# Optimization experiments

Measured on AMD Instinct MI355X. Metric: run time of the kernel, lower is better.

The kernel has to match this reference:

```python
import jax, jax.numpy as jnp
import numpy as np

B, S, D, H = 2, 2048, 1024, 16
DH = D // H
DFF = 4 * D
EPS = 1e-5


def layer_norm(x, w, b):
    m = jnp.mean(x, axis=-1, keepdims=True)
    v = jnp.mean((x - m) ** 2, axis=-1, keepdims=True)
    return (x - m) / jnp.sqrt(v + EPS) * w + b


def setup_inputs() -> dict:
    key = jax.random.key(0)
    ks = jax.random.split(key, 12)
    s = 0.02
    x = jax.random.normal(ks[0], (B, S, D), dtype=jnp.float32)
    mask = jnp.tril(jnp.ones((S, S), dtype=jnp.int32))  # causal mask, 0 = blocked
    Wq = jax.random.normal(ks[1], (H, D, DH), dtype=jnp.float32) * s
    Wk = jax.random.normal(ks[2], (H, D, DH), dtype=jnp.float32) * s
    Wv = jax.random.normal(ks[3], (H, D, DH), dtype=jnp.float32) * s
    Wo = jax.random.normal(ks[4], (D, D), dtype=jnp.float32) * s
    bo = jnp.zeros((D,), dtype=jnp.float32)
    W1 = jax.random.normal(ks[5], (D, DFF), dtype=jnp.float32) * s
    b1 = jnp.zeros((DFF,), dtype=jnp.float32)
    W2 = jax.random.normal(ks[6], (DFF, D), dtype=jnp.float32) * s
    b2 = jnp.zeros((D,), dtype=jnp.float32)
    ln1_w = jnp.ones((D,), dtype=jnp.float32)
    ln1_b = jnp.zeros((D,), dtype=jnp.float32)
    ln2_w = jnp.ones((D,), dtype=jnp.float32)
    ln2_b = jnp.zeros((D,), dtype=jnp.float32)
    return {"x": x, "mask": mask, "Wq": Wq, "Wk": Wk, "Wv": Wv, "Wo": Wo,
            "bo": bo, "W1": W1, "b1": b1, "W2": W2, "b2": b2,
            "ln1_w": ln1_w, "ln1_b": ln1_b, "ln2_w": ln2_w, "ln2_b": ln2_b}


def reference(x, mask, Wq, Wk, Wv, Wo, bo, W1, b1, W2, b2,
              ln1_w, ln1_b, ln2_w, ln2_b):
    # --- pre-LN attention ---
    xn = layer_norm(x, ln1_w, ln1_b)
    q = jnp.einsum('bsd,hdk->bhsk', xn, Wq)  # [B,H,S,DH]
    k = jnp.einsum('bsd,hdk->bhsk', xn, Wk)
    v = jnp.einsum('bsd,hdk->bhsk', xn, Wv)
    scores = jnp.einsum('bhik,bhjk->bhij', q, k) / jnp.sqrt(jnp.float32(DH))
    scores = jnp.where(mask == 0, jnp.float32(-1e9), scores)  # mask broadcasts [S,S]->[B,H,S,S]
    attn = jax.nn.softmax(scores, axis=-1)
    o = jnp.einsum('bhij,bhjk->bhik', attn, v)        # [B,H,S,DH]
    o = o.transpose(0, 2, 1, 3).reshape(x.shape[0], x.shape[1], D)  # concat heads
    attn_out = o @ Wo + bo
    x = x + attn_out
    # --- pre-LN FFN ---
    xn2 = layer_norm(x, ln2_w, ln2_b)
    h = jax.nn.relu(xn2 @ W1 + b1)
    x = x + (h @ W2 + b2)
    return x
```

## Files before the change

kernel.cpp:

```cpp
#include <hip/hip_runtime.h>
#include <hip/hip_bf16.h>
#include <stdint.h>

#define DEV static __device__ __forceinline__

using f32x4  = __attribute__((ext_vector_type(4))) float;
using bf16x4 = __attribute__((ext_vector_type(4))) __bf16;
using bf16x8 = __attribute__((ext_vector_type(8))) __bf16;

constexpr int SEQ = 2048;

DEV unsigned short f2bf(float f) {
  union { float f; unsigned u; } c; c.f = f;
  unsigned u = c.u;
  u += 0x7fffu + ((u >> 16) & 1u);
  return (unsigned short)(u >> 16);
}

DEV float wred_sum(float v) {
  #pragma unroll
  for (int m = 32; m > 0; m >>= 1) v += __shfl_xor(v, m, 64);
  return v;
}

DEV void g2l16(const unsigned short* g, unsigned short* l) {
  __builtin_amdgcn_global_load_lds(
      (const __attribute__((address_space(1))) void*)g,
      (__attribute__((address_space(3))) void*)l, 16, 0, 0);
}

DEV int xcd_map(int bid, int nwg) {
  const int cpx = nwg >> 3;
  return (bid & 7) * cpx + (bid >> 3);
}

__global__ __launch_bounds__(256) void convw_kernel(
    const float* __restrict__ in, unsigned short* __restrict__ out,
    int K, int Nh)
{
  const int h = blockIdx.z;
  const float* inh = in + (size_t)h * K * Nh;
  unsigned short* outh = out + (size_t)h * Nh * K;
  const int n0 = blockIdx.x * 32, k0 = blockIdx.y * 32;
  __shared__ float t[32][33];
  const int tx = threadIdx.x & 31, ty = threadIdx.x >> 5;
  #pragma unroll
  for (int r = 0; r < 32; r += 8)
    t[ty + r][tx] = inh[(size_t)(k0 + ty + r) * Nh + (n0 + tx)];
  __syncthreads();
  #pragma unroll
  for (int r = 0; r < 32; r += 8)
    outh[(size_t)(n0 + ty + r) * K + (k0 + tx)] = f2bf(t[tx][ty + r]);
}

__global__ __launch_bounds__(256) void ln_kernel(
    const float* __restrict__ x, const float* __restrict__ w,
    const float* __restrict__ b, unsigned short* __restrict__ out)
{
  const int row = blockIdx.x;
  const int tid = threadIdx.x;
  const float4 v = ((const float4*)(x + (size_t)row * 1024))[tid];
  float s  = v.x + v.y + v.z + v.w;
  float s2 = v.x*v.x + v.y*v.y + v.z*v.z + v.w*v.w;
  s = wred_sum(s); s2 = wred_sum(s2);
  __shared__ float rs[4], rs2[4];
  const int wave = tid >> 6, lane = tid & 63;
  if (lane == 0) { rs[wave] = s; rs2[wave] = s2; }
  __syncthreads();
  const float S  = rs[0] + rs[1] + rs[2] + rs[3];
  const float S2 = rs2[0] + rs2[1] + rs2[2] + rs2[3];
  const float mean = S * (1.f / 1024.f);
  const float var  = S2 * (1.f / 1024.f) - mean * mean;
  const float inv  = rsqrtf(var + 1e-5f);
  const float4 wv = ((const float4*)w)[tid];
  const float4 bv = ((const float4*)b)[tid];
  ushort4 o;
  o.x = f2bf((v.x - mean) * inv * wv.x + bv.x);
  o.y = f2bf((v.y - mean) * inv * wv.y + bv.y);
  o.z = f2bf((v.z - mean) * inv * wv.z + bv.z);
  o.w = f2bf((v.w - mean) * inv * wv.w + bv.w);
  ((ushort4*)(out + (size_t)row * 1024))[tid] = o;
}

template<int EPI>
__global__ __launch_bounds__(256) void gemm_kp(
    const unsigned short* __restrict__ A, const unsigned short* __restrict__ BT,
    void* __restrict__ Cout, const float* __restrict__ bias,
    const float* __restrict__ res, int M, int N, int K)
{
  __shared__ unsigned short sA[4][128 * 32];
  __shared__ unsigned short sB[4][64 * 32];
  const int tid = threadIdx.x;
  const int wave = tid >> 6, lane = tid & 63;
  const int wr = wave >> 1, wc = wave & 1;
  const int bid = xcd_map(blockIdx.y * gridDim.x + blockIdx.x, gridDim.x * gridDim.y);
  const int m0 = (bid / gridDim.x) * 128, n0 = (bid % gridDim.x) * 64;
  const int lr = lane & 15, lg = lane >> 4;
  const int wb = tid & 192;

  const f32x4 zero = {0.f, 0.f, 0.f, 0.f};
  f32x4 acc[4][2];
  #pragma unroll
  for (int i = 0; i < 4; ++i)
    #pragma unroll
    for (int j = 0; j < 2; ++j) acc[i][j] = zero;

  auto STAGE = [&](int slot, int kt) {
    const int k0 = kt * 32;
    #pragma unroll
    for (int r = 0; r < 2; ++r) {
      const int c = tid + 256 * r;
      const int row = c >> 2;
      const int so = ((c & 3) ^ ((row >> 1) & 3)) * 8;
      g2l16(A + (size_t)(m0 + row) * K + k0 + so, sA[slot] + (size_t)(r * 256 + wb) * 8);
    }
    const int row = tid >> 2;
    const int so = ((tid & 3) ^ ((row >> 1) & 3)) * 8;
    g2l16(BT + (size_t)(n0 + row) * K + k0 + so, sB[slot] + (size_t)wb * 8);
  };

  const int nt = K / 32;
  STAGE(0, 0); STAGE(1, 1); STAGE(2, 2);

  for (int t = 0; t < nt; ++t) {
    asm volatile("s_waitcnt vmcnt(6)" ::: "memory");
    __builtin_amdgcn_s_barrier();
    const int slot = t & 3;
    bf16x8 af[4], bfr[2];
    #pragma unroll
    for (int i = 0; i < 4; ++i) {
      const int row = wr * 64 + i * 16 + lr;
      af[i] = *(const bf16x8*)(sA[slot] + row * 32 + ((lg ^ ((row >> 1) & 3)) << 3));
    }
    #pragma unroll
    for (int j = 0; j < 2; ++j) {
      const int row = wc * 32 + j * 16 + lr;
      bfr[j] = *(const bf16x8*)(sB[slot] + row * 32 + ((lg ^ ((row >> 1) & 3)) << 3));
    }
    #pragma unroll
    for (int i = 0; i < 4; ++i)
      #pragma unroll
      for (int j = 0; j < 2; ++j)
        acc[i][j] = __builtin_amdgcn_mfma_f32_16x16x32_bf16(af[i], bfr[j], acc[i][j], 0, 0, 0);
    const int nx = (t + 3 < nt) ? t + 3 : nt - 1;
    STAGE((t + 3) & 3, nx);
  }
  asm volatile("s_waitcnt vmcnt(0)" ::: "memory");

  #pragma unroll
  for (int i = 0; i < 4; ++i) {
    #pragma unroll
    for (int j = 0; j < 2; ++j) {
      #pragma unroll
      for (int r = 0; r < 4; ++r) {
        const int row = m0 + wr * 64 + i * 16 + lg * 4 + r;
        const int col = n0 + wc * 32 + j * 16 + lr;
        const float v = acc[i][j][r];
        if (EPI == 1) {
          ((float*)Cout)[(size_t)row * N + col] = v + bias[col] + res[(size_t)row * N + col];
        } else {
          ((unsigned short*)Cout)[(size_t)row * N + col] = f2bf(v);
        }
      }
    }
  }
}

template<int EPI>
__global__ __launch_bounds__(512) void gemm256(
    const unsigned short* __restrict__ A, const unsigned short* __restrict__ BT,
    void* __restrict__ Cout, const float* __restrict__ bias,
    int M, int N, int K)
{
  __shared__ unsigned short sA[2][256 * 64];
  __shared__ unsigned short sB[2][256 * 64];
  const int tid = threadIdx.x;
  const int lane = tid & 63;
  const int wave = tid >> 6;
  const int wm = wave >> 2, wn = wave & 3;
  const int bid = xcd_map(blockIdx.y * gridDim.x + blockIdx.x, gridDim.x * gridDim.y);
  const int m0 = (bid / gridDim.x) * 256, n0 = (bid % gridDim.x) * 256;
  const int lr = lane & 15, lg = lane >> 4;

  const f32x4 zero = {0.f, 0.f, 0.f, 0.f};
  f32x4 acc[8][4];
  #pragma unroll
  for (int i = 0; i < 8; ++i)
    #pragma unroll
    for (int j = 0; j < 4; ++j) acc[i][j] = zero;

  auto STAGE = [&](int buf, int k0) {
    #pragma unroll
    for (int r = 0; r < 4; ++r) {
      const int c = tid + 512 * r;
      const int row = c >> 3;
      const int slot = (c & 7) ^ (row & 7);
      const int cb = (tid & 448) + 512 * r;
      g2l16(A  + (size_t)(m0 + row) * K + k0 + slot * 8, sA[buf] + (size_t)cb * 8);
      g2l16(BT + (size_t)(n0 + row) * K + k0 + slot * 8, sB[buf] + (size_t)cb * 8);
    }
  };
  auto RD = [&](const unsigned short* base, int R, int C) -> const bf16x8* {
    return (const bf16x8*)(base + R * 64 + ((((C >> 3) ^ (R & 7))) << 3));
  };

  const int nt = K / 64;
  STAGE(0, 0);
  asm volatile("s_waitcnt vmcnt(0)" ::: "memory");
  __syncthreads();

  for (int t = 0; t < nt; ++t) {
    const int buf = t & 1;
    if (t + 1 < nt) STAGE(buf ^ 1, (t + 1) * 64);
    #pragma unroll
    for (int p = 0; p < 4; ++p) {
      const int ih = p >> 1, jh = p & 1;
      bf16x8 af[4][2], bfr[2][2];
      #pragma unroll
      for (int i = 0; i < 4; ++i)
        #pragma unroll
        for (int kk = 0; kk < 2; ++kk)
          af[i][kk] = *RD(sA[buf], wm * 128 + (ih * 4 + i) * 16 + lr, kk * 32 + lg * 8);
      #pragma unroll
      for (int j = 0; j < 2; ++j)
        #pragma unroll
        for (int kk = 0; kk < 2; ++kk)
          bfr[j][kk] = *RD(sB[buf], wn * 64 + (jh * 2 + j) * 16 + lr, kk * 32 + lg * 8);
      __builtin_amdgcn_s_setprio(1);
      #pragma unroll
      for (int i = 0; i < 4; ++i)
        #pragma unroll
        for (int j = 0; j < 2; ++j)
          #pragma unroll
          for (int kk = 0; kk < 2; ++kk)
            acc[ih * 4 + i][jh * 2 + j] = __builtin_amdgcn_mfma_f32_16x16x32_bf16(
                af[i][kk], bfr[j][kk], acc[ih * 4 + i][jh * 2 + j], 0, 0, 0);
      __builtin_amdgcn_s_setprio(0);
      if (p < 3) __builtin_amdgcn_s_barrier();
    }
    asm volatile("s_waitcnt vmcnt(0)" ::: "memory");
    __builtin_amdgcn_s_barrier();
  }

  #pragma unroll
  for (int i = 0; i < 8; ++i) {
    #pragma unroll
    for (int j = 0; j < 4; ++j) {
      #pragma unroll
      for (int r = 0; r < 4; ++r) {
        const int row = m0 + wm * 128 + i * 16 + lg * 4 + r;
        const int col = n0 + wn * 64 + j * 16 + lr;
        float v = acc[i][j][r];
        if (EPI == 0) {
          if (col < 1024) v *= 0.18033688f;
          ((unsigned short*)Cout)[(size_t)row * N + col] = f2bf(v);
        } else {
          float t2 = v + bias[col];
          t2 = t2 > 0.f ? t2 : 0.f;
          ((unsigned short*)Cout)[(size_t)row * N + col] = f2bf(t2);
        }
      }
    }
  }
}

constexpr int VPAD = 136;

__global__ __launch_bounds__(512) void attn_mfma(
    const unsigned short* __restrict__ qkv, unsigned short* __restrict__ o)
{
  const int p  = blockIdx.x >> 5;
  const int bh = blockIdx.x & 31;
  const int b = bh >> 4, h = bh & 15;
  const int tid = threadIdx.x;
  const int wave = tid >> 6, lane = tid & 63;
  const int grp = wave >> 2, wv = wave & 3;
  const int lr = lane & 15, lg = lane >> 4;

  const int qi = grp ? p : (31 - p);
  const int mynt = (qi >> 1) + 1;
  const int nt_long = ((31 - p) >> 1) + 1;
  const int q0 = qi * 64;

  __shared__ unsigned short Ks[128 * 64];
  __shared__ unsigned short Vs[64 * VPAD];
  __shared__ unsigned short Ps[8][16 * VPAD];

  const size_t qbase = ((size_t)(b * SEQ + q0 + wv * 16 + lr)) * 3072 + h * 64;
  bf16x8 qb[2];
  qb[0] = *(const bf16x8*)(qkv + qbase + lg * 8);
  qb[1] = *(const bf16x8*)(qkv + qbase + 32 + lg * 8);

  const f32x4 zero = {0.f, 0.f, 0.f, 0.f};
  f32x4 o_acc[4];
  #pragma unroll
  for (int dn = 0; dn < 4; ++dn) o_acc[dn] = zero;
  float m_run = -1e30f, l_run = 0.f;

  for (int t = 0; t < nt_long; ++t) {
    const int j0 = t * 128;
    __syncthreads();
    #pragma unroll
    for (int r = 0; r < 2; ++r) {
      const int c = tid + 512 * r;
      const int row = c >> 3;
      const int slot = (c & 7) ^ (row & 7);
      const size_t gsrc = ((size_t)(b * SEQ + j0 + row)) * 3072 + 1024 + h * 64 + slot * 8;
      g2l16(qkv + gsrc, Ks + (size_t)((tid & 448) + 512 * r) * 8);
    }
    #pragma unroll
    for (int r = 0; r < 2; ++r) {
      const int c = tid + 512 * r;
      const int key = c & 127, dseg = c >> 7;
      const size_t base = ((size_t)(b * SEQ + j0 + key)) * 3072 + 2048 + h * 64 + dseg * 8;
      int4 rv = *(const int4*)(qkv + base);
      const unsigned short* u = (const unsigned short*)&rv;
      #pragma unroll
      for (int e = 0; e < 8; ++e) Vs[(dseg * 8 + e) * VPAD + key] = u[e];
    }
    __syncthreads();

    if (t < mynt) {
      f32x4 s[8];
      __builtin_amdgcn_s_setprio(1);
      #pragma unroll
      for (int n = 0; n < 8; ++n) {
        const int row = n * 16 + lr;
        const bf16x8 kf0 = *(const bf16x8*)(Ks + row * 64 + ((lg ^ (row & 7)) << 3));
        const bf16x8 kf1 = *(const bf16x8*)(Ks + row * 64 + (((4 + lg) ^ (row & 7)) << 3));
        s[n] = __builtin_amdgcn_mfma_f32_16x16x32_bf16(kf0, qb[0], zero, 0, 0, 0);
        s[n] = __builtin_amdgcn_mfma_f32_16x16x32_bf16(kf1, qb[1], s[n], 0, 0, 0);
      }
      __builtin_amdgcn_s_setprio(0);

      const bool diag = (t == mynt - 1);
      const int q = q0 + wv * 16 + lr;
      const int kbase = j0 + lg * 4;
      float zm = -3e38f;
      #pragma unroll
      for (int n = 0; n < 8; ++n)
        #pragma unroll
        for (int r = 0; r < 4; ++r) {
          float z = s[n][r];
          if (diag && (kbase + n * 16 + r > q)) z = -3e38f;
          s[n][r] = z;
          zm = fmaxf(zm, z);
        }
      zm = fmaxf(zm, __shfl_xor(zm, 16, 64));
      zm = fmaxf(zm, __shfl_xor(zm, 32, 64));
      const float mnew = fmaxf(m_run, zm);
      const float alpha = exp2f(m_run - mnew);
      m_run = mnew;
      float psum = 0.f;
      #pragma unroll
      for (int n = 0; n < 8; ++n) {
        float p0 = exp2f(s[n][0] - mnew); psum += p0;
        float p1 = exp2f(s[n][1] - mnew); psum += p1;
        float p2 = exp2f(s[n][2] - mnew); psum += p2;
        float p3 = exp2f(s[n][3] - mnew); psum += p3;
        bf16x4 pw = { (__bf16)p0, (__bf16)p1, (__bf16)p2, (__bf16)p3 };
        *(bf16x4*)(&Ps[wave][lr * VPAD + n * 16 + lg * 4]) = pw;
      }
      psum += __shfl_xor(psum, 16, 64);
      psum += __shfl_xor(psum, 32, 64);
      l_run = l_run * alpha + psum;

      float a4[4];
      #pragma unroll
      for (int r = 0; r < 4; ++r) a4[r] = __shfl(alpha, lg * 4 + r, 64);
      #pragma unroll
      for (int dn = 0; dn < 4; ++dn)
        #pragma unroll
        for (int r = 0; r < 4; ++r) o_acc[dn][r] *= a4[r];

      bf16x8 pa[4];
      #pragma unroll
      for (int kk = 0; kk < 4; ++kk)
        pa[kk] = *(const bf16x8*)(&Ps[wave][lr * VPAD + kk * 32 + lg * 8]);
      __builtin_amdgcn_s_setprio(1);
      #pragma unroll
      for (int dn = 0; dn < 4; ++dn) {
        #pragma unroll
        for (int kk = 0; kk < 4; ++kk) {
          const bf16x8 vf = *(const bf16x8*)(Vs + (dn * 16 + lr) * VPAD + kk * 32 + lg * 8);
          o_acc[dn] = __builtin_amdgcn_mfma_f32_16x16x32_bf16(pa[kk], vf, o_acc[dn], 0, 0, 0);
        }
      }
      __builtin_amdgcn_s_setprio(0);
    }
  }

  float linv[4];
  #pragma unroll
  for (int r = 0; r < 4; ++r) linv[r] = 1.f / __shfl(l_run, lg * 4 + r, 64);
  #pragma unroll
  for (int r = 0; r < 4; ++r) {
    const int qq = q0 + wv * 16 + lg * 4 + r;
    const size_t obase = ((size_t)(b * SEQ + qq)) * 1024 + h * 64;
    #pragma unroll
    for (int dn = 0; dn < 4; ++dn)
      o[obase + dn * 16 + lr] = f2bf(o_acc[dn][r] * linv[r]);
  }
}

extern "C" void kernel_launch(void* const* d_in, const int* in_sizes, int n_in,
                              void* d_out, int out_size, void* d_ws, size_t ws_size,
                              hipStream_t stream) {
  const float* x    = (const float*)d_in[0];
  const float* Wq   = (const float*)d_in[2];
  const float* Wk   = (const float*)d_in[3];
  const float* Wv   = (const float*)d_in[4];
  const float* Wo   = (const float*)d_in[5];
  const float* bo   = (const float*)d_in[6];
  const float* W1   = (const float*)d_in[7];
  const float* b1   = (const float*)d_in[8];
  const float* W2   = (const float*)d_in[9];
  const float* b2   = (const float*)d_in[10];
  const float* ln1w = (const float*)d_in[11];
  const float* ln1b = (const float*)d_in[12];
  const float* ln2w = (const float*)d_in[13];
  const float* ln2b = (const float*)d_in[14];

  char* ws = (char*)d_ws;
  unsigned short* WqkvT = (unsigned short*)(ws);
  unsigned short* WoT   = (unsigned short*)(ws + 6291456);
  unsigned short* W1T   = (unsigned short*)(ws + 8388608);
  unsigned short* W2T   = (unsigned short*)(ws + 16777216);
  unsigned short* xn    = (unsigned short*)(ws + 25165824);
  float*          x1    = (float*)        (ws + 33554432);
  unsigned short* qkv   = (unsigned short*)(ws + 50331648);
  unsigned short* oc    = (unsigned short*)(ws + 75497472);
  unsigned short* hbuf  = qkv;

  convw_kernel<<<dim3(2, 32, 16),  256, 0, stream>>>(Wq, WqkvT,               1024, 64);
  convw_kernel<<<dim3(2, 32, 16),  256, 0, stream>>>(Wk, WqkvT + 1024 * 1024, 1024, 64);
  convw_kernel<<<dim3(2, 32, 16),  256, 0, stream>>>(Wv, WqkvT + 2048 * 1024, 1024, 64);
  convw_kernel<<<dim3(32, 32, 1),  256, 0, stream>>>(Wo, WoT, 1024, 1024);
  convw_kernel<<<dim3(128, 32, 1), 256, 0, stream>>>(W1, W1T, 1024, 4096);
  convw_kernel<<<dim3(32, 128, 1), 256, 0, stream>>>(W2, W2T, 4096, 1024);

  ln_kernel<<<4096, 256, 0, stream>>>(x, ln1w, ln1b, xn);
  gemm256<0><<<dim3(12, 16), 512, 0, stream>>>(xn, WqkvT, qkv, nullptr, 4096, 3072, 1024);
  attn_mfma<<<512, 512, 0, stream>>>(qkv, oc);
  gemm_kp<1><<<dim3(16, 32), 256, 0, stream>>>(oc, WoT, x1, bo, x, 4096, 1024, 1024);
  ln_kernel<<<4096, 256, 0, stream>>>(x1, ln2w, ln2b, xn);
  gemm256<2><<<dim3(16, 16), 512, 0, stream>>>(xn, W1T, hbuf, b1, 4096, 4096, 1024);
  gemm_kp<1><<<dim3(16, 32), 256, 0, stream>>>(hbuf, W2T, (float*)d_out, b2, x1, 4096, 1024, 4096);
}
```

Baseline: 243.4 us.

## Deepen GEMM LDS pipeline and register-prefetch K/V tiles in attention

The GEMM ring buffer in shared memory grows from 4 to 6 slots, so five K-tiles are in flight and the waitcnt is adjusted to match. In attention, the direct global-to-LDS copies for K and the synchronous V loads are replaced by register prefetching: the next K/V tile is loaded into registers while the current tile is being computed, then stored into LDS at the top of the next iteration. This is meant to hide global memory latency in both kernels. The cost is more LDS in the GEMM (72KB), which may reduce occupancy, and more registers in the attention kernel.

```diff
diff --git a/kernel.cpp b/kernel.cpp
--- a/kernel.cpp
+++ b/kernel.cpp
@@ -88,8 +88,8 @@
     void* __restrict__ Cout, const float* __restrict__ bias,
     const float* __restrict__ res, int M, int N, int K)
 {
-  __shared__ unsigned short sA[4][128 * 32];
-  __shared__ unsigned short sB[4][64 * 32];
+  __shared__ unsigned short sA[6][128 * 32];
+  __shared__ unsigned short sB[6][64 * 32];
   const int tid = threadIdx.x;
   const int wave = tid >> 6, lane = tid & 63;
   const int wr = wave >> 1, wc = wave & 1;
@@ -120,12 +120,12 @@
   };
 
   const int nt = K / 32;
-  STAGE(0, 0); STAGE(1, 1); STAGE(2, 2);
+  STAGE(0, 0); STAGE(1, 1); STAGE(2, 2); STAGE(3, 3); STAGE(4, 4);
 
   for (int t = 0; t < nt; ++t) {
-    asm volatile("s_waitcnt vmcnt(6)" ::: "memory");
+    asm volatile("s_waitcnt vmcnt(12)" ::: "memory");
     __builtin_amdgcn_s_barrier();
-    const int slot = t & 3;
+    const int slot = t % 6;
     bf16x8 af[4], bfr[2];
     #pragma unroll
     for (int i = 0; i < 4; ++i) {
@@ -142,8 +142,8 @@
       #pragma unroll
       for (int j = 0; j < 2; ++j)
         acc[i][j] = __builtin_amdgcn_mfma_f32_16x16x32_bf16(af[i], bfr[j], acc[i][j], 0, 0, 0);
-    const int nx = (t + 3 < nt) ? t + 3 : nt - 1;
-    STAGE((t + 3) & 3, nx);
+    const int nx = (t + 5 < nt) ? t + 5 : nt - 1;
+    STAGE((t + 5) % 6, nx);
   }
   asm volatile("s_waitcnt vmcnt(0)" ::: "memory");
 
@@ -297,30 +297,36 @@
   for (int dn = 0; dn < 4; ++dn) o_acc[dn] = zero;
   float m_run = -1e30f, l_run = 0.f;
 
+  const int c0 = tid, c1 = tid + 512;
+  const int krow0 = c0 >> 3, ksg0 = c0 & 7, krow1 = c1 >> 3, ksg1 = c1 & 7;
+  const int vkey0 = c0 & 127, vds0 = c0 >> 7, vkey1 = c1 & 127, vds1 = c1 >> 7;
+
+  int4 kreg[2], vreg[2];
+  auto LOADKV = [&](int j0) {
+    kreg[0] = *(const int4*)(qkv + ((size_t)(b * SEQ + j0 + krow0)) * 3072 + 1024 + h * 64 + ksg0 * 8);
+    kreg[1] = *(const int4*)(qkv + ((size_t)(b * SEQ + j0 + krow1)) * 3072 + 1024 + h * 64 + ksg1 * 8);
+    vreg[0] = *(const int4*)(qkv + ((size_t)(b * SEQ + j0 + vkey0)) * 3072 + 2048 + h * 64 + vds0 * 8);
+    vreg[1] = *(const int4*)(qkv + ((size_t)(b * SEQ + j0 + vkey1)) * 3072 + 2048 + h * 64 + vds1 * 8);
+  };
+
+  LOADKV(0);
   for (int t = 0; t < nt_long; ++t) {
-    const int j0 = t * 128;
+    *(int4*)(Ks + krow0 * 64 + ((ksg0 ^ (krow0 & 7)) << 3)) = kreg[0];
+    *(int4*)(Ks + krow1 * 64 + ((ksg1 ^ (krow1 & 7)) << 3)) = kreg[1];
+    {
+      const unsigned short* u0 = (const unsigned short*)&vreg[0];
+      const unsigned short* u1 = (const unsigned short*)&vreg[1];
+      #pragma unroll
+      for (int e = 0; e < 8; ++e) {
+        Vs[(vds0 * 8 + e) * VPAD + vkey0] = u0[e];
+        Vs[(vds1 * 8 + e) * VPAD + vkey1] = u1[e];
+      }
+    }
     __syncthreads();
-    #pragma unroll
-    for (int r = 0; r < 2; ++r) {
-      const int c = tid + 512 * r;
-      const int row = c >> 3;
-      const int slot = (c & 7) ^ (row & 7);
-      const size_t gsrc = ((size_t)(b * SEQ + j0 + row)) * 3072 + 1024 + h * 64 + slot * 8;
-      g2l16(qkv + gsrc, Ks + (size_t)((tid & 448) + 512 * r) * 8);
-    }
-    #pragma unroll
-    for (int r = 0; r < 2; ++r) {
-      const int c = tid + 512 * r;
-      const int key = c & 127, dseg = c >> 7;
-      const size_t base = ((size_t)(b * SEQ + j0 + key)) * 3072 + 2048 + h * 64 + dseg * 8;
-      int4 rv = *(const int4*)(qkv + base);
-      const unsigned short* u = (const unsigned short*)&rv;
-      #pragma unroll
-      for (int e = 0; e < 8; ++e) Vs[(dseg * 8 + e) * VPAD + key] = u[e];
-    }
-    __syncthreads();
+    if (t + 1 < nt_long) LOADKV((t + 1) * 128);
 
     if (t < mynt) {
+      const int j0 = t * 128;
       f32x4 s[8];
       __builtin_amdgcn_s_setprio(1);
       #pragma unroll
@@ -388,6 +394,7 @@
       }
       __builtin_amdgcn_s_setprio(0);
     }
+    __syncthreads();
   }
 
   float linv[4];
```

Measured after the change: 251.7 us. 1.03x slower.

## Deepen K tile to 64 with 3-stage pipeline and MFMA priority boost

Applied to the files above, without the earlier changes.

The projection GEMM kernel now stages 64-wide K tiles instead of 32-wide, using 3 LDS buffers and a prefetch distance of two tiles instead of four buffers and three. Each iteration issues twice as many MFMAs per barrier and uses an 8-way XOR swizzle for the wider rows. MFMA sections are wrapped in s_setprio to favour compute issue. The goal is fewer barriers and loop iterations per unit of work. The cost is more LDS per block (72KB vs 48KB), which may lower occupancy, and the vmcnt(6) wait now matches the 6 loads per stage.

```diff
diff --git a/kernel.cpp b/kernel.cpp
--- a/kernel.cpp
+++ b/kernel.cpp
@@ -88,8 +88,8 @@
     void* __restrict__ Cout, const float* __restrict__ bias,
     const float* __restrict__ res, int M, int N, int K)
 {
-  __shared__ unsigned short sA[4][128 * 32];
-  __shared__ unsigned short sB[4][64 * 32];
+  __shared__ unsigned short sA[3][128 * 64];
+  __shared__ unsigned short sB[3][64 * 64];
   const int tid = threadIdx.x;
   const int wave = tid >> 6, lane = tid & 63;
   const int wr = wave >> 1, wc = wave & 1;
@@ -106,44 +106,56 @@
     for (int j = 0; j < 2; ++j) acc[i][j] = zero;
 
   auto STAGE = [&](int slot, int kt) {
-    const int k0 = kt * 32;
+    const int k0 = kt * 64;
+    #pragma unroll
+    for (int r = 0; r < 4; ++r) {
+      const int c = tid + 256 * r;
+      const int row = c >> 3;
+      const int so = ((c & 7) ^ (row & 7)) * 8;
+      g2l16(A + (size_t)(m0 + row) * K + k0 + so, sA[slot] + (size_t)(wb + 256 * r) * 8);
+    }
     #pragma unroll
     for (int r = 0; r < 2; ++r) {
       const int c = tid + 256 * r;
-      const int row = c >> 2;
-      const int so = ((c & 3) ^ ((row >> 1) & 3)) * 8;
-      g2l16(A + (size_t)(m0 + row) * K + k0 + so, sA[slot] + (size_t)(r * 256 + wb) * 8);
-    }
-    const int row = tid >> 2;
-    const int so = ((tid & 3) ^ ((row >> 1) & 3)) * 8;
-    g2l16(BT + (size_t)(n0 + row) * K + k0 + so, sB[slot] + (size_t)wb * 8);
+      const int row = c >> 3;
+      const int so = ((c & 7) ^ (row & 7)) * 8;
+      g2l16(BT + (size_t)(n0 + row) * K + k0 + so, sB[slot] + (size_t)(wb + 256 * r) * 8);
+    }
   };
 
-  const int nt = K / 32;
-  STAGE(0, 0); STAGE(1, 1); STAGE(2, 2);
+  const int nt = K / 64;
+  STAGE(0, 0); STAGE(1, 1);
 
   for (int t = 0; t < nt; ++t) {
     asm volatile("s_waitcnt vmcnt(6)" ::: "memory");
     __builtin_amdgcn_s_barrier();
-    const int slot = t & 3;
-    bf16x8 af[4], bfr[2];
+    const int slot = t % 3;
+    bf16x8 af[4][2], bfr[2][2];
     #pragma unroll
     for (int i = 0; i < 4; ++i) {
       const int row = wr * 64 + i * 16 + lr;
-      af[i] = *(const bf16x8*)(sA[slot] + row * 32 + ((lg ^ ((row >> 1) & 3)) << 3));
+      #pragma unroll
+      for (int kk = 0; kk < 2; ++kk)
+        af[i][kk] = *(const bf16x8*)(sA[slot] + row * 64 + (((kk * 4 + lg) ^ (row & 7)) << 3));
     }
     #pragma unroll
     for (int j = 0; j < 2; ++j) {
       const int row = wc * 32 + j * 16 + lr;
-      bfr[j] = *(const bf16x8*)(sB[slot] + row * 32 + ((lg ^ ((row >> 1) & 3)) << 3));
-    }
+      #pragma unroll
+      for (int kk = 0; kk < 2; ++kk)
+        bfr[j][kk] = *(const bf16x8*)(sB[slot] + row * 64 + (((kk * 4 + lg) ^ (row & 7)) << 3));
+    }
+    __builtin_amdgcn_s_setprio(1);
     #pragma unroll
     for (int i = 0; i < 4; ++i)
       #pragma unroll
       for (int j = 0; j < 2; ++j)
-        acc[i][j] = __builtin_amdgcn_mfma_f32_16x16x32_bf16(af[i], bfr[j], acc[i][j], 0, 0, 0);
-    const int nx = (t + 3 < nt) ? t + 3 : nt - 1;
-    STAGE((t + 3) & 3, nx);
+        #pragma unroll
+        for (int kk = 0; kk < 2; ++kk)
+          acc[i][j] = __builtin_amdgcn_mfma_f32_16x16x32_bf16(af[i][kk], bfr[j][kk], acc[i][j], 0, 0, 0);
+    __builtin_amdgcn_s_setprio(0);
+    const int nx = (t + 2 < nt) ? t + 2 : nt - 1;
+    STAGE((t + 2) % 3, nx);
   }
   asm volatile("s_waitcnt vmcnt(0)" ::: "memory");
 
```

After: 240.5 us. Within noise of the previous version (-1.2%).
